# Performance work log

Measured on AMD Instinct MI355X. Metric: run time of the kernel, lower is better.

Reference implementation:

```python
import jax, jax.numpy as jnp
import numpy as np

B, DM, H, W = 2, 96, 48, 48
E = 192          # d_expand == d_inner
R, N = 6, 16     # delta_rank, d_state


def conv2d(x, w, b, groups=1, pad=0):
    out = jax.lax.conv_general_dilated(
        x, w, window_strides=(1, 1), padding=[(pad, pad), (pad, pad)],
        dimension_numbers=("NCHW", "OIHW", "NCHW"), feature_group_count=groups)
    return out + b[None, :, None, None]


def setup_inputs() -> dict:
    key = jax.random.key(0)
    ks = jax.random.split(key, 24)
    f = lambda k, shape, s: jax.random.normal(k, shape, jnp.float32) * s
    inp = {
        "x": jax.random.normal(ks[0], (B, DM, H, W), jnp.float32),
        "in_proj_w": f(ks[1], (2 * E, DM), 0.05),
        "conv_w": f(ks[2], (E, 1, 3, 3), 0.2),
        "conv_b": f(ks[3], (E,), 0.1),
        "x_proj_w": f(ks[4], (4, R + 2 * N, E), 0.01),
        "dt_proj_w": f(ks[5], (4, E, R), 0.01),
        "dt_proj_b": jnp.full((4, E), -9.0) + f(ks[6], (4, E), 0.1),
        "A_log": jnp.tile(jnp.log(jnp.arange(1, N + 1, dtype=jnp.float32))[None, None, :], (4, E, 1)),
        "Ds": jnp.ones((4, E), jnp.float32),
        "ln_g": jnp.ones(E, jnp.float32), "ln_b": jnp.zeros(E, jnp.float32),
        "c1_w": f(ks[7], (2 * E, E, 1, 1), 0.05), "c1_b": jnp.zeros(2 * E),
        "bn1_g": jnp.ones(2 * E), "bn1_b": jnp.zeros(2 * E), "bn1_m": jnp.zeros(2 * E), "bn1_v": jnp.ones(2 * E),
        "c2_w": f(ks[8], (2 * E, 1, 3, 3), 0.2), "c2_b": jnp.zeros(2 * E),
        "bn2_g": jnp.ones(2 * E), "bn2_b": jnp.zeros(2 * E), "bn2_m": jnp.zeros(2 * E), "bn2_v": jnp.ones(2 * E),
        "c3_w": f(ks[9], (E // 2, 2 * E, 1, 1), 0.05), "c3_b": jnp.zeros(E // 2),
        "se1_w": f(ks[10], (E // 4, E // 2), 0.1), "se1_b": jnp.zeros(E // 4),
        "se2_w": f(ks[11], (E // 2, E // 4), 0.1), "se2_b": jnp.zeros(E // 2),
    }
    return inp


def reference(x, in_proj_w, conv_w, conv_b, x_proj_w, dt_proj_w, dt_proj_b,
              A_log, Ds, ln_g, ln_b,
              c1_w, c1_b, bn1_g, bn1_b, bn1_m, bn1_v,
              c2_w, c2_b, bn2_g, bn2_b, bn2_m, bn2_v,
              c3_w, c3_b, se1_w, se1_b, se2_w, se2_b):
    Bs, _, Hs, Ws = x.shape
    L = Hs * Ws
    # in projection (Linear over channel dim), split x/z gates
    xz = jnp.einsum("bchw,oc->bohw", x, in_proj_w)
    xi, z = jnp.split(xz, 2, axis=1)
    # depthwise conv + SiLU
    xi = jax.nn.silu(conv2d(xi, conv_w, conv_b, groups=E, pad=1))
    # ---- selective scan (4-direction cross scan, cumsum formulation) ----
    xf = xi.reshape(Bs, E, L)
    xt = jnp.swapaxes(xi, 2, 3).reshape(Bs, E, L)
    xs = jnp.stack([xf, xf[..., ::-1], xt, xt[..., ::-1]], axis=1)  # [B,4,E,L]
    dbc = jnp.einsum("bkcl,krc->bkrl", xs, x_proj_w)                # [B,4,R+2N,L]
    dlt, b, c = dbc[:, :, :R], dbc[:, :, R:R + N], dbc[:, :, R + N:]
    dlt = jnp.einsum("bkrl,kdr->bkdl", dlt, dt_proj_w) + dt_proj_b[None, :, :, None]
    dlt = jax.nn.softplus(dlt)                                      # [B,4,E,L]
    dA = dlt[..., None] * A_log[None, :, :, None, :]                # [B,4,E,L,N]
    phi = jnp.exp(-jnp.cumsum(dA, axis=3))
    dbx = dlt[..., None] * jnp.swapaxes(b, 2, 3)[:, :, None] * xs[..., None]  # [B,4,E,L,N]
    h = phi * jnp.cumsum(dbx / (phi + 1e-12), axis=3)
    y = jnp.einsum("bkdln,bknl->bkdl", h, c) + Ds[None, :, :, None]  # [B,4,E,L]
    # ---- cross merge ----
    y1 = y[:, 0]
    y2 = y[:, 1, :, ::-1]
    y3 = jnp.swapaxes(y[:, 2].reshape(Bs, E, Ws, Hs), 2, 3).reshape(Bs, E, L)
    y4 = jnp.swapaxes(y[:, 3, :, ::-1].reshape(Bs, E, Ws, Hs), 2, 3).reshape(Bs, E, L)
    ys = (y1 + y2 + y3 + y4).reshape(Bs, E, Hs, Ws)
    # layernorm over channels
    yn = jnp.moveaxis(ys, 1, -1)
    mu = yn.mean(-1, keepdims=True)
    var = yn.var(-1, keepdims=True)
    yn = (yn - mu) / jnp.sqrt(var + 1e-5) * ln_g + ln_b
    u = jnp.moveaxis(yn, -1, 1) * z
    # ---- EFFN ----
    def bn(t, g, bb, m, v):
        return (t - m[None, :, None, None]) / jnp.sqrt(v + 1e-5)[None, :, None, None] * g[None, :, None, None] + bb[None, :, None, None]
    t = jax.nn.relu(bn(conv2d(u, c1_w, c1_b), bn1_g, bn1_b, bn1_m, bn1_v))
    t = jax.nn.relu(bn(conv2d(t, c2_w, c2_b, groups=2 * E, pad=1), bn2_g, bn2_b, bn2_m, bn2_v))
    t = conv2d(t, c3_w, c3_b)
    # squeeze-excitation: t + t * sigmoid(fc(relu(fc(avgpool(t)))))
    s = t.mean((2, 3))
    s = jax.nn.relu(s @ se1_w.T + se1_b)
    s = jax.nn.sigmoid(s @ se2_w.T + se2_b)
    return t + t * s[:, :, None, None]
```

## Files before the change

kernel.cpp:

```cpp
#include <hip/hip_runtime.h>
#include <hip/hip_bf16.h>

#define LTOT 2304
#define ECH  192
#define NCH  16
#define CCH  96
#define SCH  24

__device__ __forceinline__ int permS(int k, int l) {
  if (k == 0) return l;
  if (k == 1) return LTOT - 1 - l;
  int m = (k == 2) ? l : (LTOT - 1 - l);
  return (m % 48) * 48 + (m / 48);
}

__device__ __forceinline__ float softplusf(float x) {
  return (x > 20.f) ? x : log1pf(__expf(x));
}

__global__ __launch_bounds__(256) void k1_inproj(const float* __restrict__ x,
                                                 const float* __restrict__ W,
                                                 float* __restrict__ xi_pre,
                                                 float* __restrict__ z) {
  const int l0 = blockIdx.x * 64;
  const int o0 = blockIdx.y * 64;
  const int b  = blockIdx.z;
  __shared__ __align__(16) float xs[64 * 97];
  __shared__ __align__(16) float Wl[96 * 68];
  const int tid = threadIdx.x;
  for (int idx = tid; idx < 96 * 64; idx += 256) {
    int i = idx & 63, c = idx >> 6;
    xs[i * 97 + c] = x[(b * 96 + c) * LTOT + l0 + i];
  }
  for (int idx = tid; idx < 64 * 96; idx += 256) {
    int r = idx / 96, c = idx - r * 96;
    Wl[c * 68 + r] = W[(o0 + r) * 96 + c];
  }
  __syncthreads();
  const int lane = tid & 63, w = tid >> 6;
  const int jj = lane & 15, rq = lane >> 4;
  const int rbase = 16 * w + 4 * rq;
  float acc[4][4];
#pragma unroll
  for (int p = 0; p < 4; ++p)
#pragma unroll
    for (int t = 0; t < 4; ++t) acc[p][t] = 0.f;
#pragma unroll 2
  for (int c = 0; c < 96; ++c) {
    const float4 wv = *(const float4*)&Wl[c * 68 + rbase];
    float xv[4];
#pragma unroll
    for (int p = 0; p < 4; ++p) xv[p] = xs[(jj + 16 * p) * 97 + c];
#pragma unroll
    for (int p = 0; p < 4; ++p) {
      acc[p][0] = fmaf(wv.x, xv[p], acc[p][0]);
      acc[p][1] = fmaf(wv.y, xv[p], acc[p][1]);
      acc[p][2] = fmaf(wv.z, xv[p], acc[p][2]);
      acc[p][3] = fmaf(wv.w, xv[p], acc[p][3]);
    }
  }
  __syncthreads();
  float* ol = xs;
#pragma unroll
  for (int p = 0; p < 4; ++p)
#pragma unroll
    for (int t = 0; t < 4; ++t) ol[(rbase + t) * 65 + jj + 16 * p] = acc[p][t];
  __syncthreads();
  for (int idx = tid; idx < 64 * 64; idx += 256) {
    int r = idx & 63, pos = idx >> 6;
    float v = ol[r * 65 + pos];
    int o = o0 + r, l = l0 + pos;
    if (o < ECH) xi_pre[(b * LTOT + l) * ECH + o] = v;
    else         z[(b * LTOT + l) * ECH + (o - ECH)] = v;
  }
}

__global__ __launch_bounds__(256) void k2_dwconv(const float* __restrict__ xi_pre,
                                                 const float* __restrict__ cw,
                                                 const float* __restrict__ cb,
                                                 float* __restrict__ xi) {
  int g = blockIdx.x * 256 + threadIdx.x;
  if (g >= 2 * LTOT * ECH) return;
  int e = g % ECH; int l = (g / ECH) % LTOT; int b = g / (ECH * LTOT);
  int h = l / 48, wq = l % 48;
  float acc = cb[e];
#pragma unroll
  for (int kh = 0; kh < 3; ++kh) {
    int hh = h + kh - 1; if (hh < 0 || hh >= 48) continue;
#pragma unroll
    for (int kw = 0; kw < 3; ++kw) {
      int ww = wq + kw - 1; if (ww < 0 || ww >= 48) continue;
      acc = fmaf(cw[e * 9 + kh * 3 + kw], xi_pre[(b * LTOT + hh * 48 + ww) * ECH + e], acc);
    }
  }
  xi[g] = acc / (1.f + __expf(-acc));
}

__global__ __launch_bounds__(256) void k3_xproj(const float* __restrict__ xi,
                                                const float* __restrict__ xw,
                                                const float* __restrict__ dtw,
                                                const float* __restrict__ dtb,
                                                float* __restrict__ dlt,
                                                float* __restrict__ bT,
                                                float* __restrict__ cT) {
  const int l0 = blockIdx.x * 32;
  const int k  = blockIdx.y;
  const int b  = blockIdx.z;
  __shared__ __align__(16) float xs[32 * 193];
  __shared__ __align__(16) float Wl[192 * 40];
  __shared__ float dl6[6 * 33];
  const int tid = threadIdx.x;
  for (int idx = tid; idx < 32 * 192; idx += 256) {
    int j = idx / 192, c = idx - j * 192;
    int s = permS(k, l0 + j);
    xs[j * 193 + c] = xi[(b * LTOT + s) * ECH + c];
  }
  const float* wsrc = xw + k * 38 * ECH;
  for (int idx = tid; idx < 38 * 192; idx += 256) {
    int r = idx / 192, c = idx - r * 192;
    Wl[c * 40 + r] = wsrc[idx];
  }
  __syncthreads();
  const int lane = tid & 63, w = tid >> 6;
  const int jj = lane & 15;
  const int rq = w * 4 + (lane >> 4);
  const int rqc = rq < 9 ? rq : 9;
  const int j0 = 2 * jj;
  float a00 = 0.f, a01 = 0.f, a02 = 0.f, a03 = 0.f;
  float a10 = 0.f, a11 = 0.f, a12 = 0.f, a13 = 0.f;
#pragma unroll 4
  for (int c = 0; c < 192; ++c) {
    float x0 = xs[j0 * 193 + c];
    float x1 = xs[j0 * 193 + 193 + c];
    const float4 wv = *(const float4*)&Wl[c * 40 + 4 * rqc];
    a00 = fmaf(wv.x, x0, a00); a01 = fmaf(wv.y, x0, a01);
    a02 = fmaf(wv.z, x0, a02); a03 = fmaf(wv.w, x0, a03);
    a10 = fmaf(wv.x, x1, a10); a11 = fmaf(wv.y, x1, a11);
    a12 = fmaf(wv.z, x1, a12); a13 = fmaf(wv.w, x1, a13);
  }
  const int bk = b * 4 + k;
  if (rq < 10) {
    float av[2][4] = {{a00, a01, a02, a03}, {a10, a11, a12, a13}};
#pragma unroll
    for (int t = 0; t < 4; ++t) {
      int r = 4 * rq + t;
      if (r >= 38) continue;
#pragma unroll
      for (int p = 0; p < 2; ++p) {
        int j = j0 + p;
        float v = av[p][t];
        if (r < 6)       dl6[r * 33 + j] = v;
        else if (r < 22) bT[((bk * LTOT) + l0 + j) * NCH + (r - 6)] = v;
        else             cT[((bk * LTOT) + l0 + j) * NCH + (r - 22)] = v;
      }
    }
  }
  __syncthreads();
  for (int idx = tid; idx < 32 * 192; idx += 256) {
    int j = idx / 192, d = idx - j * 192;
    float a = dtb[k * ECH + d];
    const float* wd = dtw + (k * ECH + d) * 6;
#pragma unroll
    for (int r = 0; r < 6; ++r) a = fmaf(wd[r], dl6[r * 33 + j], a);
    dlt[((bk * LTOT) + l0 + j) * ECH + d] = softplusf(a);
  }
}

__global__ __launch_bounds__(256) void k4a_scan1(const float* __restrict__ dlt,
                                                 const float* __restrict__ xi,
                                                 const float* __restrict__ bT,
                                                 const float* __restrict__ Alog,
                                                 float* __restrict__ q,
                                                 float* __restrict__ Ts) {
  const int cb = blockIdx.x;
  const int db = blockIdx.y;
  const int bk = blockIdx.z;
  const int b = bk >> 2, k = bk & 3;
  const int l0 = cb * 96;
  __shared__ float sdl[96 * 64];
  __shared__ float sxi[96 * 64];
  __shared__ __align__(16) float sb[96 * NCH];
  const int tid = threadIdx.x;
  const int dd = tid & 63, cg = tid >> 6;
  const int dg = db * 64 + dd;
  for (int j = cg; j < 96; j += 4) {
    sdl[j * 64 + dd] = dlt[(bk * LTOT + l0 + j) * ECH + dg];
    int s = permS(k, l0 + j);
    sxi[j * 64 + dd] = xi[(b * LTOT + s) * ECH + dg];
  }
  for (int idx = tid; idx < 96 * NCH; idx += 256) sb[idx] = bT[(bk * LTOT + l0) * NCH + idx];
  __syncthreads();
  float C1[16], C2[16], C3[16], h[16];
#pragma unroll
  for (int n = 0; n < 16; ++n) {
    float a = Alog[(k * ECH + dg) * NCH + n];
    C1[n] = a; C2[n] = 0.5f * a * a; C3[n] = (1.f / 6.f) * a * a * a;
    h[n] = 0.f;
  }
  float Tsum = 0.f;
  const int c = cb * 4 + cg;
  for (int i = 0; i < SCH; ++i) {
    int j = cg * SCH + i;
    float dl = sdl[j * 64 + dd];
    float u  = dl * sxi[j * 64 + dd];
    Tsum += dl;
    const float4* bb4 = (const float4*)(sb + j * NCH);
    float4 q0 = bb4[0], q1 = bb4[1], q2 = bb4[2], q3 = bb4[3];
    float bbl[16] = {q0.x, q0.y, q0.z, q0.w, q1.x, q1.y, q1.z, q1.w,
                     q2.x, q2.y, q2.z, q2.w, q3.x, q3.y, q3.z, q3.w};
    if (dl <= 0.018f) {
#pragma unroll
      for (int n = 0; n < 16; ++n) {
        float e = fmaf(dl, fmaf(dl, fmaf(dl, -C3[n], C2[n]), -C1[n]), 1.f);
        h[n] = fmaf(e, h[n], u * bbl[n]);
      }
    } else {
#pragma unroll
      for (int n = 0; n < 16; ++n) {
        float e = __expf(-C1[n] * dl);
        h[n] = fmaf(e, h[n], u * bbl[n]);
      }
    }
  }
  float* qp = q + ((bk * CCH + c) * ECH + dg) * NCH;
#pragma unroll
  for (int n = 0; n < 16; ++n) qp[n] = h[n];
  Ts[(bk * CCH + c) * ECH + dg] = Tsum;
}

__global__ __launch_bounds__(256) void k4b_comb(const float* __restrict__ Alog,
                                                const float* __restrict__ Ts,
                                                float* __restrict__ q) {
  int t = blockIdx.x * 256 + threadIdx.x;
  if (t >= 8 * ECH * NCH) return;
  int n = t & 15, d = (t >> 4) % ECH, bk = t / (NCH * ECH);
  int k = bk & 3;
  float A = Alog[(k * ECH + d) * NCH + n];
  float h = 0.f;
  for (int c = 0; c < CCH; ++c) {
    int base = ((bk * CCH + c) * ECH + d) * NCH + n;
    float qc = q[base];
    q[base] = h;
    float xv = A * Ts[(bk * CCH + c) * ECH + d];
    float P = (xv <= 0.05f)
                  ? fmaf(xv, fmaf(xv, fmaf(xv, -(1.f / 6.f), 0.5f), -1.f), 1.f)
                  : __expf(-xv);
    h = fmaf(P, h, qc);
  }
}

__global__ __launch_bounds__(256) void k4c_scan2(const float* __restrict__ dlt,
                                                 const float* __restrict__ xi,
                                                 const float* __restrict__ bT,
                                                 const float* __restrict__ cT,
                                                 const float* __restrict__ Alog,
                                                 const float* __restrict__ hin,
                                                 float* __restrict__ ys) {
  const int cb = blockIdx.x;
  const int db = blockIdx.y;
  const int bk = blockIdx.z;
  const int b = bk >> 2, k = bk & 3;
  const int l0 = cb * 96;
  __shared__ float sdl[96 * 64];
  __shared__ float sxi[96 * 64];
  __shared__ __align__(16) float sb[96 * NCH];
  __shared__ __align__(16) float sc[96 * NCH];
  const int tid = threadIdx.x;
  const int dd = tid & 63, cg = tid >> 6;
  const int dg = db * 64 + dd;
  for (int j = cg; j < 96; j += 4) {
    sdl[j * 64 + dd] = dlt[(bk * LTOT + l0 + j) * ECH + dg];
    int s = permS(k, l0 + j);
    sxi[j * 64 + dd] = xi[(b * LTOT + s) * ECH + dg];
  }
  for (int idx = tid; idx < 96 * NCH; idx += 256) {
    sb[idx] = bT[(bk * LTOT + l0) * NCH + idx];
    sc[idx] = cT[(bk * LTOT + l0) * NCH + idx];
  }
  __syncthreads();
  float C1[16], C2[16], C3[16], h[16];
  const int c = cb * 4 + cg;
  const float* hp = hin + ((bk * CCH + c) * ECH + dg) * NCH;
#pragma unroll
  for (int n = 0; n < 16; ++n) {
    float a = Alog[(k * ECH + dg) * NCH + n];
    C1[n] = a; C2[n] = 0.5f * a * a; C3[n] = (1.f / 6.f) * a * a * a;
    h[n] = hp[n];
  }
  for (int i = 0; i < SCH; ++i) {
    int j = cg * SCH + i;
    int l = l0 + j;
    float dl = sdl[j * 64 + dd];
    float u  = dl * sxi[j * 64 + dd];
    const float4* bb4 = (const float4*)(sb + j * NCH);
    float4 q0 = bb4[0], q1 = bb4[1], q2 = bb4[2], q3 = bb4[3];
    float bbl[16] = {q0.x, q0.y, q0.z, q0.w, q1.x, q1.y, q1.z, q1.w,
                     q2.x, q2.y, q2.z, q2.w, q3.x, q3.y, q3.z, q3.w};
    if (dl <= 0.018f) {
#pragma unroll
      for (int n = 0; n < 16; ++n) {
        float e = fmaf(dl, fmaf(dl, fmaf(dl, -C3[n], C2[n]), -C1[n]), 1.f);
        h[n] = fmaf(e, h[n], u * bbl[n]);
      }
    } else {
#pragma unroll
      for (int n = 0; n < 16; ++n) {
        float e = __expf(-C1[n] * dl);
        h[n] = fmaf(e, h[n], u * bbl[n]);
      }
    }
    const float4* cc4 = (const float4*)(sc + j * NCH);
    float4 c0 = cc4[0], c1 = cc4[1], c2 = cc4[2], c3 = cc4[3];
    float ccl[16] = {c0.x, c0.y, c0.z, c0.w, c1.x, c1.y, c1.z, c1.w,
                     c2.x, c2.y, c2.z, c2.w, c3.x, c3.y, c3.z, c3.w};
    float y = 0.f;
#pragma unroll
    for (int n = 0; n < 16; ++n) y = fmaf(h[n], ccl[n], y);
    int s = permS(k, l);
    atomicAdd(&ys[(b * LTOT + s) * ECH + dg], y);
  }
}

__global__ __launch_bounds__(256) void k5_ln(const float* __restrict__ ys,
                                             const float* __restrict__ Ds,
                                             const float* __restrict__ lng,
                                             const float* __restrict__ lnb,
                                             float* __restrict__ zu) {
  int p = blockIdx.x * 4 + (threadIdx.x >> 6);
  int lane = threadIdx.x & 63;
  const float* yp = ys + p * ECH;
  float vd[3], sd[3];
#pragma unroll
  for (int t = 0; t < 3; ++t) {
    int d = lane + t * 64;
    vd[t] = yp[d];
    sd[t] = Ds[d] + Ds[ECH + d] + Ds[2 * ECH + d] + Ds[3 * ECH + d];
  }
  float s1 = vd[0] + vd[1] + vd[2];
  float s2 = sd[0] + sd[1] + sd[2];
#pragma unroll
  for (int off = 32; off > 0; off >>= 1) {
    s1 += __shfl_xor(s1, off, 64);
    s2 += __shfl_xor(s2, off, 64);
  }
  float mean_dot = s1 * (1.f / 192.f);
  float mean_sd  = s2 * (1.f / 192.f);
  float dev[3];
  float ss = 0.f;
#pragma unroll
  for (int t = 0; t < 3; ++t) {
    dev[t] = (vd[t] - mean_dot) + (sd[t] - mean_sd);
    ss = fmaf(dev[t], dev[t], ss);
  }
#pragma unroll
  for (int off = 32; off > 0; off >>= 1) ss += __shfl_xor(ss, off, 64);
  float rstd = 1.f / sqrtf(ss * (1.f / 192.f) + 1e-5f);
#pragma unroll
  for (int t = 0; t < 3; ++t) {
    int d = lane + t * 64;
    float yn = (dev[t] * rstd) * lng[d] + lnb[d];
    zu[p * ECH + d] = yn * zu[p * ECH + d];
  }
}

__global__ __launch_bounds__(256) void k6_c1(const float* __restrict__ u,
                                             const float* __restrict__ W,
                                             const float* __restrict__ c1b,
                                             const float* __restrict__ g1,
                                             const float* __restrict__ b1,
                                             const float* __restrict__ m1,
                                             const float* __restrict__ v1,
                                             float* __restrict__ t1) {
  const int l0 = blockIdx.x * 64;
  const int o0 = blockIdx.y * 64;
  const int b  = blockIdx.z;
  __shared__ __align__(16) float xs[64 * 97];
  __shared__ __align__(16) float Wl[96 * 68];
  const int tid = threadIdx.x;
  const int lane = tid & 63, w = tid >> 6;
  const int jj = lane & 15, rq = lane >> 4;
  const int rbase = 16 * w + 4 * rq;
  float acc[4][4];
#pragma unroll
  for (int p = 0; p < 4; ++p)
#pragma unroll
    for (int t = 0; t < 4; ++t) acc[p][t] = 0.f;
  for (int kc = 0; kc < 2; ++kc) {
    if (kc) __syncthreads();
    for (int idx = tid; idx < 64 * 96; idx += 256) {
      int i = idx / 96, c = idx - i * 96;
      xs[i * 97 + c] = u[(b * LTOT + l0 + i) * ECH + kc * 96 + c];
    }
    for (int idx = tid; idx < 64 * 96; idx += 256) {
      int r = idx / 96, c = idx - r * 96;
      Wl[c * 68 + r] = W[(o0 + r) * ECH + kc * 96 + c];
    }
    __syncthreads();
#pragma unroll 2
    for (int c = 0; c < 96; ++c) {
      const float4 wv = *(const float4*)&Wl[c * 68 + rbase];
      float xv[4];
#pragma unroll
      for (int p = 0; p < 4; ++p) xv[p] = xs[(jj + 16 * p) * 97 + c];
#pragma unroll
      for (int p = 0; p < 4; ++p) {
        acc[p][0] = fmaf(wv.x, xv[p], acc[p][0]);
        acc[p][1] = fmaf(wv.y, xv[p], acc[p][1]);
        acc[p][2] = fmaf(wv.z, xv[p], acc[p][2]);
        acc[p][3] = fmaf(wv.w, xv[p], acc[p][3]);
      }
    }
  }
#pragma unroll
  for (int t = 0; t < 4; ++t) {
    int o = o0 + rbase + t;
    float sc = g1[o] / sqrtf(v1[o] + 1e-5f);
    float bias = (c1b[o] - m1[o]) * sc + b1[o];
#pragma unroll
    for (int p = 0; p < 4; ++p) acc[p][t] = fmaxf(fmaf(acc[p][t], sc, bias), 0.f);
  }
  __syncthreads();
  float* ol = xs;
#pragma unroll
  for (int p = 0; p < 4; ++p)
#pragma unroll
    for (int t = 0; t < 4; ++t) ol[(rbase + t) * 65 + jj + 16 * p] = acc[p][t];
  __syncthreads();
  for (int idx = tid; idx < 64 * 64; idx += 256) {
    int pos = idx & 63, r = idx >> 6;
    t1[(b * 384 + o0 + r) * LTOT + l0 + pos] = ol[r * 65 + pos];
  }
}

__global__ __launch_bounds__(256) void k7_dw2(const float* __restrict__ t1,
                                              const float* __restrict__ cw,
                                              const float* __restrict__ cb,
                                              const float* __restrict__ g2,
                                              const float* __restrict__ b2,
                                              const float* __restrict__ m2,
                                              const float* __restrict__ v2,
                                              float* __restrict__ t2) {
  int g = blockIdx.x * 256 + threadIdx.x;
  if (g >= 2 * LTOT * 384) return;
  int l = g % LTOT; int o = (g / LTOT) % 384; int b = g / (LTOT * 384);
  int h = l / 48, wq = l % 48;
  const float* src = t1 + (b * 384 + o) * LTOT;
  float acc = cb[o];
#pragma unroll
  for (int kh = 0; kh < 3; ++kh) {
    int hh = h + kh - 1; if (hh < 0 || hh >= 48) continue;
#pragma unroll
    for (int kw = 0; kw < 3; ++kw) {
      int ww = wq + kw - 1; if (ww < 0 || ww >= 48) continue;
      acc = fmaf(cw[o * 9 + kh * 3 + kw], src[hh * 48 + ww], acc);
    }
  }
  float sc = g2[o] / sqrtf(v2[o] + 1e-5f);
  float val = (acc - m2[o]) * sc + b2[o];
  t2[g] = fmaxf(val, 0.f);
}

__global__ __launch_bounds__(256) void k8_c3(const float* __restrict__ t2,
                                             const float* __restrict__ W,
                                             const float* __restrict__ c3b,
                                             float* __restrict__ t3,
                                             float* __restrict__ se) {
  const int l0 = blockIdx.x * 64;
  const int r0 = blockIdx.y * 32;
  const int b  = blockIdx.z;
  __shared__ __align__(16) float xs[64 * 97];
  __shared__ __align__(16) float Wl[96 * 36];
  const int tid = threadIdx.x;
  const int lane = tid & 63, w = tid >> 6;
  const int jj = lane & 15, rq = lane >> 4;
  const int rloc = 8 * w + 2 * rq;
  float acc[4][2];
#pragma unroll
  for (int p = 0; p < 4; ++p) { acc[p][0] = 0.f; acc[p][1] = 0.f; }
  for (int kc = 0; kc < 4; ++kc) {
    if (kc) __syncthreads();
    for (int idx = tid; idx < 64 * 96; idx += 256) {
      int i = idx & 63, c = idx >> 6;
      xs[i * 97 + c] = t2[(b * 384 + kc * 96 + c) * LTOT + l0 + i];
    }
    for (int idx = tid; idx < 32 * 96; idx += 256) {
      int r = idx / 96, c = idx - r * 96;
      Wl[c * 36 + r] = W[(r0 + r) * 384 + kc * 96 + c];
    }
    __syncthreads();
#pragma unroll 2
    for (int c = 0; c < 96; ++c) {
      const float2 wv = *(const float2*)&Wl[c * 36 + rloc];
      float xv[4];
#pragma unroll
      for (int p = 0; p < 4; ++p) xv[p] = xs[(jj + 16 * p) * 97 + c];
#pragma unroll
      for (int p = 0; p < 4; ++p) {
        acc[p][0] = fmaf(wv.x, xv[p], acc[p][0]);
        acc[p][1] = fmaf(wv.y, xv[p], acc[p][1]);
      }
    }
  }
#pragma unroll
  for (int t = 0; t < 2; ++t) {
    float bias = c3b[r0 + rloc + t];
#pragma unroll
    for (int p = 0; p < 4; ++p) acc[p][t] += bias;
  }
#pragma unroll
  for (int t = 0; t < 2; ++t) {
    float v = acc[0][t] + acc[1][t] + acc[2][t] + acc[3][t];
    v += __shfl_xor(v, 1); v += __shfl_xor(v, 2);
    v += __shfl_xor(v, 4); v += __shfl_xor(v, 8);
    if (jj == 0) atomicAdd(&se[b * 96 + r0 + rloc + t], v);
  }
  __syncthreads();
  float* ol = xs;
#pragma unroll
  for (int p = 0; p < 4; ++p)
#pragma unroll
    for (int t = 0; t < 2; ++t) ol[(rloc + t) * 65 + jj + 16 * p] = acc[p][t];
  __syncthreads();
  for (int idx = tid; idx < 32 * 64; idx += 256) {
    int pos = idx & 63, r = idx >> 6;
    t3[(b * 96 + r0 + r) * LTOT + l0 + pos] = ol[r * 65 + pos];
  }
}

__global__ __launch_bounds__(256) void k9a_se(const float* __restrict__ se,
                                              const float* __restrict__ w1,
                                              const float* __restrict__ sb1,
                                              const float* __restrict__ w2,
                                              const float* __restrict__ sb2,
                                              float* __restrict__ smul) {
  __shared__ float sm[192];
  __shared__ float s1[96];
  int t = threadIdx.x;
  if (t < 192) sm[t] = se[t] * (1.f / 2304.f);
  __syncthreads();
  if (t < 96) {
    int b = t / 48, i = t % 48;
    float acc = sb1[i];
    for (int m = 0; m < 96; ++m) acc = fmaf(w1[i * 96 + m], sm[b * 96 + m], acc);
    s1[t] = fmaxf(acc, 0.f);
  }
  __syncthreads();
  if (t < 192) {
    int b = t / 96, j = t % 96;
    float acc = sb2[j];
    for (int i = 0; i < 48; ++i) acc = fmaf(w2[j * 48 + i], s1[b * 48 + i], acc);
    smul[t] = 1.f + 1.f / (1.f + __expf(-acc));
  }
}

__global__ __launch_bounds__(256) void k9b_out(const float* __restrict__ t3,
                                               const float* __restrict__ smul,
                                               float* __restrict__ out) {
  int g = blockIdx.x * 256 + threadIdx.x;
  if (g >= 2 * 96 * LTOT) return;
  int bj = g / LTOT;
  out[g] = t3[g] * smul[bj];
}

extern "C" void kernel_launch(void* const* d_in, const int* in_sizes, int n_in,
                              void* d_out, int out_size, void* d_ws, size_t ws_size,
                              hipStream_t stream) {
  const float* x     = (const float*)d_in[0];
  const float* inw   = (const float*)d_in[1];
  const float* convw = (const float*)d_in[2];
  const float* convb = (const float*)d_in[3];
  const float* xpw   = (const float*)d_in[4];
  const float* dtw   = (const float*)d_in[5];
  const float* dtb   = (const float*)d_in[6];
  const float* Alog  = (const float*)d_in[7];
  const float* Ds    = (const float*)d_in[8];
  const float* lng   = (const float*)d_in[9];
  const float* lnb   = (const float*)d_in[10];
  const float* c1w   = (const float*)d_in[11];
  const float* c1b   = (const float*)d_in[12];
  const float* bn1g  = (const float*)d_in[13];
  const float* bn1b  = (const float*)d_in[14];
  const float* bn1m  = (const float*)d_in[15];
  const float* bn1v  = (const float*)d_in[16];
  const float* c2w   = (const float*)d_in[17];
  const float* c2b   = (const float*)d_in[18];
  const float* bn2g  = (const float*)d_in[19];
  const float* bn2b  = (const float*)d_in[20];
  const float* bn2m  = (const float*)d_in[21];
  const float* bn2v  = (const float*)d_in[22];
  const float* c3w   = (const float*)d_in[23];
  const float* c3b   = (const float*)d_in[24];
  const float* se1w  = (const float*)d_in[25];
  const float* se1b  = (const float*)d_in[26];
  const float* se2w  = (const float*)d_in[27];
  const float* se2b  = (const float*)d_in[28];

  float* ws = (float*)d_ws;
  float* xi_pre = ws;
  float* z      = ws + 884736;
  float* xi     = ws + 1769472;
  float* dlt    = ws + 2654208;
  float* bT     = ws + 6193152;
  float* cT     = ws + 6782976;
  float* ys     = ws + 7372800;
  float* q      = ws + 8257536;
  float* Ts     = ws + 10616832;
  float* se     = ws + 10764288;
  float* smul   = ws + 10764480;
  float* t1 = dlt;
  float* t2 = dlt + 1769472;
  float* t3 = cT;

  hipMemsetAsync(ys, 0, 884736 * sizeof(float), stream);
  hipMemsetAsync(se, 0, 192 * sizeof(float), stream);

  k1_inproj<<<dim3(36, 6, 2), 256, 0, stream>>>(x, inw, xi_pre, z);
  k2_dwconv<<<3456, 256, 0, stream>>>(xi_pre, convw, convb, xi);
  k3_xproj<<<dim3(72, 4, 2), 256, 0, stream>>>(xi, xpw, dtw, dtb, dlt, bT, cT);
  k4a_scan1<<<dim3(24, 3, 8), 256, 0, stream>>>(dlt, xi, bT, Alog, q, Ts);
  k4b_comb<<<96, 256, 0, stream>>>(Alog, Ts, q);
  k4c_scan2<<<dim3(24, 3, 8), 256, 0, stream>>>(dlt, xi, bT, cT, Alog, q, ys);
  k5_ln<<<1152, 256, 0, stream>>>(ys, Ds, lng, lnb, z);
  k6_c1<<<dim3(36, 6, 2), 256, 0, stream>>>(z, c1w, c1b, bn1g, bn1b, bn1m, bn1v, t1);
  k7_dw2<<<6912, 256, 0, stream>>>(t1, c2w, c2b, bn2g, bn2b, bn2m, bn2v, t2);
  k8_c3<<<dim3(36, 3, 2), 256, 0, stream>>>(t2, c3w, c3b, t3, se);
  k9a_se<<<1, 256, 0, stream>>>(se, se1w, se1b, se2w, se2b, smul);
  k9b_out<<<1728, 256, 0, stream>>>(t3, smul, (float*)d_out);
}
```

Baseline: 349.4 us.

## Recompute delta in scan kernels, drop memsets, transpose GEMM smem tiles

The x-projection kernel now writes only the rank-6 delta inputs. Both scan kernels recompute dt_proj plus softplus on the fly instead of reading a full [B,4,L,E] delta tensor, which cuts a large global write and two reads. The scan now writes per-direction outputs (yd) rather than atomically accumulating into a zeroed ys, so the ys memset goes away, and the SE accumulator is zeroed inside k6. The GEMM kernels switch their shared-memory input tiles to a channel-major layout with float2 loads, and q/h are moved with float4. The cost is redundant softplus and exp work across the two scan passes and a changed scan staging scheme split into halves.

```diff
diff --git a/kernel.cpp b/kernel.cpp
--- a/kernel.cpp
+++ b/kernel.cpp
@@ -14,8 +14,9 @@
   return (m % 48) * 48 + (m / 48);
 }
 
-__device__ __forceinline__ float softplusf(float x) {
-  return (x > 20.f) ? x : log1pf(__expf(x));
+__device__ __forceinline__ float sp_fast(float x) {
+  float t = __expf(x);
+  return (t <= 0.018f) ? t * fmaf(t, fmaf(t, 0.33333334f, -0.5f), 1.f) : log1pf(t);
 }
 
 __global__ __launch_bounds__(256) void k1_inproj(const float* __restrict__ x,
@@ -25,46 +26,49 @@
   const int l0 = blockIdx.x * 64;
   const int o0 = blockIdx.y * 64;
   const int b  = blockIdx.z;
-  __shared__ __align__(16) float xs[64 * 97];
+  __shared__ __align__(16) float xs[96 * 66];
   __shared__ __align__(16) float Wl[96 * 68];
   const int tid = threadIdx.x;
   for (int idx = tid; idx < 96 * 64; idx += 256) {
-    int i = idx & 63, c = idx >> 6;
-    xs[i * 97 + c] = x[(b * 96 + c) * LTOT + l0 + i];
+    int i = idx & 63, cc = idx >> 6;
+    xs[cc * 66 + i] = x[(b * 96 + cc) * LTOT + l0 + i];
   }
   for (int idx = tid; idx < 64 * 96; idx += 256) {
-    int r = idx / 96, c = idx - r * 96;
-    Wl[c * 68 + r] = W[(o0 + r) * 96 + c];
+    int r = idx / 96, cc = idx - r * 96;
+    Wl[cc * 68 + r] = W[(o0 + r) * 96 + cc];
   }
   __syncthreads();
   const int lane = tid & 63, w = tid >> 6;
-  const int jj = lane & 15, rq = lane >> 4;
-  const int rbase = 16 * w + 4 * rq;
+  const int jj = lane & 15, rqq = lane >> 4;
+  const int rbase = 16 * w + 4 * rqq;
   float acc[4][4];
 #pragma unroll
   for (int p = 0; p < 4; ++p)
 #pragma unroll
     for (int t = 0; t < 4; ++t) acc[p][t] = 0.f;
 #pragma unroll 2
-  for (int c = 0; c < 96; ++c) {
-    const float4 wv = *(const float4*)&Wl[c * 68 + rbase];
-    float xv[4];
-#pragma unroll
-    for (int p = 0; p < 4; ++p) xv[p] = xs[(jj + 16 * p) * 97 + c];
-#pragma unroll
-    for (int p = 0; p < 4; ++p) {
-      acc[p][0] = fmaf(wv.x, xv[p], acc[p][0]);
-      acc[p][1] = fmaf(wv.y, xv[p], acc[p][1]);
-      acc[p][2] = fmaf(wv.z, xv[p], acc[p][2]);
-      acc[p][3] = fmaf(wv.w, xv[p], acc[p][3]);
-    }
+  for (int cc = 0; cc < 96; ++cc) {
+    const float4 wv = *(const float4*)&Wl[cc * 68 + rbase];
+    const float2 xa = *(const float2*)&xs[cc * 66 + 2 * jj];
+    const float2 xb = *(const float2*)&xs[cc * 66 + 32 + 2 * jj];
+    acc[0][0] = fmaf(wv.x, xa.x, acc[0][0]); acc[0][1] = fmaf(wv.y, xa.x, acc[0][1]);
+    acc[0][2] = fmaf(wv.z, xa.x, acc[0][2]); acc[0][3] = fmaf(wv.w, xa.x, acc[0][3]);
+    acc[1][0] = fmaf(wv.x, xa.y, acc[1][0]); acc[1][1] = fmaf(wv.y, xa.y, acc[1][1]);
+    acc[1][2] = fmaf(wv.z, xa.y, acc[1][2]); acc[1][3] = fmaf(wv.w, xa.y, acc[1][3]);
+    acc[2][0] = fmaf(wv.x, xb.x, acc[2][0]); acc[2][1] = fmaf(wv.y, xb.x, acc[2][1]);
+    acc[2][2] = fmaf(wv.z, xb.x, acc[2][2]); acc[2][3] = fmaf(wv.w, xb.x, acc[2][3]);
+    acc[3][0] = fmaf(wv.x, xb.y, acc[3][0]); acc[3][1] = fmaf(wv.y, xb.y, acc[3][1]);
+    acc[3][2] = fmaf(wv.z, xb.y, acc[3][2]); acc[3][3] = fmaf(wv.w, xb.y, acc[3][3]);
   }
   __syncthreads();
   float* ol = xs;
 #pragma unroll
-  for (int p = 0; p < 4; ++p)
-#pragma unroll
-    for (int t = 0; t < 4; ++t) ol[(rbase + t) * 65 + jj + 16 * p] = acc[p][t];
+  for (int t = 0; t < 4; ++t) {
+    ol[(rbase + t) * 65 + 2 * jj]      = acc[0][t];
+    ol[(rbase + t) * 65 + 2 * jj + 1]  = acc[1][t];
+    ol[(rbase + t) * 65 + 2 * jj + 32] = acc[2][t];
+    ol[(rbase + t) * 65 + 2 * jj + 33] = acc[3][t];
+  }
   __syncthreads();
   for (int idx = tid; idx < 64 * 64; idx += 256) {
     int r = idx & 63, pos = idx >> 6;
@@ -98,29 +102,20 @@
 
 __global__ __launch_bounds__(256) void k3_xproj(const float* __restrict__ xi,
                                                 const float* __restrict__ xw,
-                                                const float* __restrict__ dtw,
-                                                const float* __restrict__ dtb,
-                                                float* __restrict__ dlt,
+                                                float* __restrict__ dl6g,
                                                 float* __restrict__ bT,
                                                 float* __restrict__ cT) {
   const int l0 = blockIdx.x * 32;
   const int k  = blockIdx.y;
   const int b  = blockIdx.z;
-  __shared__ __align__(16) float xs[32 * 193];
+  __shared__ __align__(16) float xs[96 * 34];
   __shared__ __align__(16) float Wl[192 * 40];
-  __shared__ float dl6[6 * 33];
   const int tid = threadIdx.x;
-  for (int idx = tid; idx < 32 * 192; idx += 256) {
-    int j = idx / 192, c = idx - j * 192;
-    int s = permS(k, l0 + j);
-    xs[j * 193 + c] = xi[(b * LTOT + s) * ECH + c];
-  }
   const float* wsrc = xw + k * 38 * ECH;
   for (int idx = tid; idx < 38 * 192; idx += 256) {
-    int r = idx / 192, c = idx - r * 192;
-    Wl[c * 40 + r] = wsrc[idx];
-  }
-  __syncthreads();
+    int r = idx / 192, cc = idx - r * 192;
+    Wl[cc * 40 + r] = wsrc[idx];
+  }
   const int lane = tid & 63, w = tid >> 6;
   const int jj = lane & 15;
   const int rq = w * 4 + (lane >> 4);
@@ -128,15 +123,23 @@
   const int j0 = 2 * jj;
   float a00 = 0.f, a01 = 0.f, a02 = 0.f, a03 = 0.f;
   float a10 = 0.f, a11 = 0.f, a12 = 0.f, a13 = 0.f;
+  for (int kc = 0; kc < 2; ++kc) {
+    __syncthreads();
+    for (int idx = tid; idx < 32 * 96; idx += 256) {
+      int j = idx / 96, cc = idx - j * 96;
+      int s = permS(k, l0 + j);
+      xs[cc * 34 + j] = xi[(b * LTOT + s) * ECH + kc * 96 + cc];
+    }
+    __syncthreads();
 #pragma unroll 4
-  for (int c = 0; c < 192; ++c) {
-    float x0 = xs[j0 * 193 + c];
-    float x1 = xs[j0 * 193 + 193 + c];
-    const float4 wv = *(const float4*)&Wl[c * 40 + 4 * rqc];
-    a00 = fmaf(wv.x, x0, a00); a01 = fmaf(wv.y, x0, a01);
-    a02 = fmaf(wv.z, x0, a02); a03 = fmaf(wv.w, x0, a03);
-    a10 = fmaf(wv.x, x1, a10); a11 = fmaf(wv.y, x1, a11);
-    a12 = fmaf(wv.z, x1, a12); a13 = fmaf(wv.w, x1, a13);
+    for (int cc = 0; cc < 96; ++cc) {
+      const float2 xv = *(const float2*)&xs[cc * 34 + j0];
+      const float4 wv = *(const float4*)&Wl[(kc * 96 + cc) * 40 + 4 * rqc];
+      a00 = fmaf(wv.x, xv.x, a00); a01 = fmaf(wv.y, xv.x, a01);
+      a02 = fmaf(wv.z, xv.x, a02); a03 = fmaf(wv.w, xv.x, a03);
+      a10 = fmaf(wv.x, xv.y, a10); a11 = fmaf(wv.y, xv.y, a11);
+      a12 = fmaf(wv.z, xv.y, a12); a13 = fmaf(wv.w, xv.y, a13);
+    }
   }
   const int bk = b * 4 + k;
   if (rq < 10) {
@@ -149,27 +152,20 @@
       for (int p = 0; p < 2; ++p) {
         int j = j0 + p;
         float v = av[p][t];
-        if (r < 6)       dl6[r * 33 + j] = v;
+        if (r < 6)       dl6g[((bk * LTOT) + l0 + j) * 6 + r] = v;
         else if (r < 22) bT[((bk * LTOT) + l0 + j) * NCH + (r - 6)] = v;
         else             cT[((bk * LTOT) + l0 + j) * NCH + (r - 22)] = v;
       }
     }
   }
-  __syncthreads();
-  for (int idx = tid; idx < 32 * 192; idx += 256) {
-    int j = idx / 192, d = idx - j * 192;
-    float a = dtb[k * ECH + d];
-    const float* wd = dtw + (k * ECH + d) * 6;
-#pragma unroll
-    for (int r = 0; r < 6; ++r) a = fmaf(wd[r], dl6[r * 33 + j], a);
-    dlt[((bk * LTOT) + l0 + j) * ECH + d] = softplusf(a);
-  }
-}
-
-__global__ __launch_bounds__(256) void k4a_scan1(const float* __restrict__ dlt,
+}
+
+__global__ __launch_bounds__(256) void k4a_scan1(const float* __restrict__ dl6g,
                                                  const float* __restrict__ xi,
                                                  const float* __restrict__ bT,
                                                  const float* __restrict__ Alog,
+                                                 const float* __restrict__ dtw,
+                                                 const float* __restrict__ dtb,
                                                  float* __restrict__ q,
                                                  float* __restrict__ Ts) {
   const int cb = blockIdx.x;
@@ -177,54 +173,75 @@
   const int bk = blockIdx.z;
   const int b = bk >> 2, k = bk & 3;
   const int l0 = cb * 96;
-  __shared__ float sdl[96 * 64];
-  __shared__ float sxi[96 * 64];
-  __shared__ __align__(16) float sb[96 * NCH];
+  __shared__ __align__(16) float2 sdx[48 * 64];
+  __shared__ __align__(16) float  sb[96 * NCH];
+  __shared__ __align__(16) float  sdl6[96 * 6];
   const int tid = threadIdx.x;
   const int dd = tid & 63, cg = tid >> 6;
   const int dg = db * 64 + dd;
-  for (int j = cg; j < 96; j += 4) {
-    sdl[j * 64 + dd] = dlt[(bk * LTOT + l0 + j) * ECH + dg];
-    int s = permS(k, l0 + j);
-    sxi[j * 64 + dd] = xi[(b * LTOT + s) * ECH + dg];
-  }
+  float b6 = dtb[k * ECH + dg];
+  float w6[6];
+  {
+    const float2* d2 = (const float2*)(dtw + (k * ECH + dg) * 6);
+    float2 u0 = d2[0], u1 = d2[1], u2 = d2[2];
+    w6[0] = u0.x; w6[1] = u0.y; w6[2] = u1.x; w6[3] = u1.y; w6[4] = u2.x; w6[5] = u2.y;
+  }
+  for (int idx = tid; idx < 96 * 6; idx += 256) sdl6[idx] = dl6g[(bk * LTOT + l0) * 6 + idx];
   for (int idx = tid; idx < 96 * NCH; idx += 256) sb[idx] = bT[(bk * LTOT + l0) * NCH + idx];
-  __syncthreads();
-  float C1[16], C2[16], C3[16], h[16];
+  float C1[16], h[16];
 #pragma unroll
   for (int n = 0; n < 16; ++n) {
-    float a = Alog[(k * ECH + dg) * NCH + n];
-    C1[n] = a; C2[n] = 0.5f * a * a; C3[n] = (1.f / 6.f) * a * a * a;
+    C1[n] = Alog[(k * ECH + dg) * NCH + n];
     h[n] = 0.f;
   }
   float Tsum = 0.f;
   const int c = cb * 4 + cg;
-  for (int i = 0; i < SCH; ++i) {
-    int j = cg * SCH + i;
-    float dl = sdl[j * 64 + dd];
-    float u  = dl * sxi[j * 64 + dd];
-    Tsum += dl;
-    const float4* bb4 = (const float4*)(sb + j * NCH);
-    float4 q0 = bb4[0], q1 = bb4[1], q2 = bb4[2], q3 = bb4[3];
-    float bbl[16] = {q0.x, q0.y, q0.z, q0.w, q1.x, q1.y, q1.z, q1.w,
-                     q2.x, q2.y, q2.z, q2.w, q3.x, q3.y, q3.z, q3.w};
-    if (dl <= 0.018f) {
-#pragma unroll
-      for (int n = 0; n < 16; ++n) {
-        float e = fmaf(dl, fmaf(dl, fmaf(dl, -C3[n], C2[n]), -C1[n]), 1.f);
-        h[n] = fmaf(e, h[n], u * bbl[n]);
+  for (int half = 0; half < 2; ++half) {
+    __syncthreads();
+    for (int e = tid; e < 48 * 64; e += 256) {
+      int s = e >> 6;
+      int j = (s / 12) * 24 + half * 12 + (s % 12);
+      const float* d6 = sdl6 + j * 6;
+      float xa = b6;
+#pragma unroll
+      for (int r = 0; r < 6; ++r) xa = fmaf(w6[r], d6[r], xa);
+      float dl = sp_fast(xa);
+      int sp = permS(k, l0 + j);
+      float xiv = xi[(b * LTOT + sp) * ECH + dg];
+      sdx[s * 64 + dd] = make_float2(dl, xiv);
+    }
+    __syncthreads();
+    for (int i = 0; i < 12; ++i) {
+      int j = cg * 24 + half * 12 + i;
+      float2 dx = sdx[(cg * 12 + i) * 64 + dd];
+      float dl = dx.x;
+      float u  = dl * dx.y;
+      Tsum += dl;
+      const float4* bb4 = (const float4*)(sb + j * NCH);
+      float4 q0 = bb4[0], q1 = bb4[1], q2 = bb4[2], q3 = bb4[3];
+      float bbl[16] = {q0.x, q0.y, q0.z, q0.w, q1.x, q1.y, q1.z, q1.w,
+                       q2.x, q2.y, q2.z, q2.w, q3.x, q3.y, q3.z, q3.w};
+      if (dl <= 0.018f) {
+#pragma unroll
+        for (int n = 0; n < 16; ++n) {
+          float xn = C1[n] * dl;
+          float e = fmaf(xn, fmaf(xn, fmaf(xn, -(1.f / 6.f), 0.5f), -1.f), 1.f);
+          h[n] = fmaf(e, h[n], u * bbl[n]);
+        }
+      } else {
+#pragma unroll
+        for (int n = 0; n < 16; ++n) {
+          float e = __expf(-C1[n] * dl);
+          h[n] = fmaf(e, h[n], u * bbl[n]);
+        }
       }
-    } else {
-#pragma unroll
-      for (int n = 0; n < 16; ++n) {
-        float e = __expf(-C1[n] * dl);
-        h[n] = fmaf(e, h[n], u * bbl[n]);
-      }
-    }
-  }
-  float* qp = q + ((bk * CCH + c) * ECH + dg) * NCH;
-#pragma unroll
-  for (int n = 0; n < 16; ++n) qp[n] = h[n];
+    }
+  }
+  float4* qp = (float4*)(q + ((bk * CCH + c) * ECH + dg) * NCH);
+  qp[0] = make_float4(h[0], h[1], h[2], h[3]);
+  qp[1] = make_float4(h[4], h[5], h[6], h[7]);
+  qp[2] = make_float4(h[8], h[9], h[10], h[11]);
+  qp[3] = make_float4(h[12], h[13], h[14], h[15]);
   Ts[(bk * CCH + c) * ECH + dg] = Tsum;
 }
 
@@ -249,91 +266,118 @@
   }
 }
 
-__global__ __launch_bounds__(256) void k4c_scan2(const float* __restrict__ dlt,
+__global__ __launch_bounds__(256) void k4c_scan2(const float* __restrict__ dl6g,
                                                  const float* __restrict__ xi,
                                                  const float* __restrict__ bT,
                                                  const float* __restrict__ cT,
                                                  const float* __restrict__ Alog,
+                                                 const float* __restrict__ dtw,
+                                                 const float* __restrict__ dtb,
                                                  const float* __restrict__ hin,
-                                                 float* __restrict__ ys) {
+                                                 float* __restrict__ yd) {
   const int cb = blockIdx.x;
   const int db = blockIdx.y;
   const int bk = blockIdx.z;
   const int b = bk >> 2, k = bk & 3;
   const int l0 = cb * 96;
-  __shared__ float sdl[96 * 64];
-  __shared__ float sxi[96 * 64];
-  __shared__ __align__(16) float sb[96 * NCH];
-  __shared__ __align__(16) float sc[96 * NCH];
+  __shared__ __align__(16) float2 sdx[48 * 64];
+  __shared__ __align__(16) float  sb[96 * NCH];
+  __shared__ __align__(16) float  sc[96 * NCH];
+  __shared__ __align__(16) float  sdl6[96 * 6];
   const int tid = threadIdx.x;
   const int dd = tid & 63, cg = tid >> 6;
   const int dg = db * 64 + dd;
-  for (int j = cg; j < 96; j += 4) {
-    sdl[j * 64 + dd] = dlt[(bk * LTOT + l0 + j) * ECH + dg];
-    int s = permS(k, l0 + j);
-    sxi[j * 64 + dd] = xi[(b * LTOT + s) * ECH + dg];
-  }
+  float b6 = dtb[k * ECH + dg];
+  float w6[6];
+  {
+    const float2* d2 = (const float2*)(dtw + (k * ECH + dg) * 6);
+    float2 u0 = d2[0], u1 = d2[1], u2 = d2[2];
+    w6[0] = u0.x; w6[1] = u0.y; w6[2] = u1.x; w6[3] = u1.y; w6[4] = u2.x; w6[5] = u2.y;
+  }
+  for (int idx = tid; idx < 96 * 6; idx += 256) sdl6[idx] = dl6g[(bk * LTOT + l0) * 6 + idx];
   for (int idx = tid; idx < 96 * NCH; idx += 256) {
     sb[idx] = bT[(bk * LTOT + l0) * NCH + idx];
     sc[idx] = cT[(bk * LTOT + l0) * NCH + idx];
   }
-  __syncthreads();
-  float C1[16], C2[16], C3[16], h[16];
+  float C1[16], h[16];
   const int c = cb * 4 + cg;
-  const float* hp = hin + ((bk * CCH + c) * ECH + dg) * NCH;
-#pragma unroll
-  for (int n = 0; n < 16; ++n) {
-    float a = Alog[(k * ECH + dg) * NCH + n];
-    C1[n] = a; C2[n] = 0.5f * a * a; C3[n] = (1.f / 6.f) * a * a * a;
-    h[n] = hp[n];
-  }
-  for (int i = 0; i < SCH; ++i) {
-    int j = cg * SCH + i;
-    int l = l0 + j;
-    float dl = sdl[j * 64 + dd];
-    float u  = dl * sxi[j * 64 + dd];
-    const float4* bb4 = (const float4*)(sb + j * NCH);
-    float4 q0 = bb4[0], q1 = bb4[1], q2 = bb4[2], q3 = bb4[3];
-    float bbl[16] = {q0.x, q0.y, q0.z, q0.w, q1.x, q1.y, q1.z, q1.w,
-                     q2.x, q2.y, q2.z, q2.w, q3.x, q3.y, q3.z, q3.w};
-    if (dl <= 0.018f) {
-#pragma unroll
-      for (int n = 0; n < 16; ++n) {
-        float e = fmaf(dl, fmaf(dl, fmaf(dl, -C3[n], C2[n]), -C1[n]), 1.f);
-        h[n] = fmaf(e, h[n], u * bbl[n]);
+  const float4* hp = (const float4*)(hin + ((bk * CCH + c) * ECH + dg) * NCH);
+  {
+    float4 h0 = hp[0], h1 = hp[1], h2 = hp[2], h3 = hp[3];
+    h[0]=h0.x; h[1]=h0.y; h[2]=h0.z; h[3]=h0.w;
+    h[4]=h1.x; h[5]=h1.y; h[6]=h1.z; h[7]=h1.w;
+    h[8]=h2.x; h[9]=h2.y; h[10]=h2.z; h[11]=h2.w;
+    h[12]=h3.x; h[13]=h3.y; h[14]=h3.z; h[15]=h3.w;
+  }
+#pragma unroll
+  for (int n = 0; n < 16; ++n) C1[n] = Alog[(k * ECH + dg) * NCH + n];
+  float* ydk = yd + (b * 4 + k) * LTOT * ECH;
+  for (int half = 0; half < 2; ++half) {
+    __syncthreads();
+    for (int e = tid; e < 48 * 64; e += 256) {
+      int s = e >> 6;
+      int j = (s / 12) * 24 + half * 12 + (s % 12);
+      const float* d6 = sdl6 + j * 6;
+      float xa = b6;
+#pragma unroll
+      for (int r = 0; r < 6; ++r) xa = fmaf(w6[r], d6[r], xa);
+      float dl = sp_fast(xa);
+      int sp = permS(k, l0 + j);
+      float xiv = xi[(b * LTOT + sp) * ECH + dg];
+      sdx[s * 64 + dd] = make_float2(dl, xiv);
+    }
+    __syncthreads();
+    for (int i = 0; i < 12; ++i) {
+      int j = cg * 24 + half * 12 + i;
+      float2 dx = sdx[(cg * 12 + i) * 64 + dd];
+      float dl = dx.x;
+      float u  = dl * dx.y;
+      const float4* bb4 = (const float4*)(sb + j * NCH);
+      float4 q0 = bb4[0], q1 = bb4[1], q2 = bb4[2], q3 = bb4[3];
+      float bbl[16] = {q0.x, q0.y, q0.z, q0.w, q1.x, q1.y, q1.z, q1.w,
+                       q2.x, q2.y, q2.z, q2.w, q3.x, q3.y, q3.z, q3.w};
+      if (dl <= 0.018f) {
+#pragma unroll
+        for (int n = 0; n < 16; ++n) {
+          float xn = C1[n] * dl;
+          float e = fmaf(xn, fmaf(xn, fmaf(xn, -(1.f / 6.f), 0.5f), -1.f), 1.f);
+          h[n] = fmaf(e, h[n], u * bbl[n]);
+        }
+      } else {
+#pragma unroll
+        for (int n = 0; n < 16; ++n) {
+          float e = __expf(-C1[n] * dl);
+          h[n] = fmaf(e, h[n], u * bbl[n]);
+        }
       }
-    } else {
-#pragma unroll
-      for (int n = 0; n < 16; ++n) {
-        float e = __expf(-C1[n] * dl);
-        h[n] = fmaf(e, h[n], u * bbl[n]);
-      }
-    }
-    const float4* cc4 = (const float4*)(sc + j * NCH);
-    float4 c0 = cc4[0], c1 = cc4[1], c2 = cc4[2], c3 = cc4[3];
-    float ccl[16] = {c0.x, c0.y, c0.z, c0.w, c1.x, c1.y, c1.z, c1.w,
-                     c2.x, c2.y, c2.z, c2.w, c3.x, c3.y, c3.z, c3.w};
-    float y = 0.f;
-#pragma unroll
-    for (int n = 0; n < 16; ++n) y = fmaf(h[n], ccl[n], y);
-    int s = permS(k, l);
-    atomicAdd(&ys[(b * LTOT + s) * ECH + dg], y);
-  }
-}
-
-__global__ __launch_bounds__(256) void k5_ln(const float* __restrict__ ys,
+      const float4* cc4 = (const float4*)(sc + j * NCH);
+      float4 c0 = cc4[0], c1 = cc4[1], c2 = cc4[2], c3 = cc4[3];
+      float ccl[16] = {c0.x, c0.y, c0.z, c0.w, c1.x, c1.y, c1.z, c1.w,
+                       c2.x, c2.y, c2.z, c2.w, c3.x, c3.y, c3.z, c3.w};
+      float y = 0.f;
+#pragma unroll
+      for (int n = 0; n < 16; ++n) y = fmaf(h[n], ccl[n], y);
+      int sp = permS(k, l0 + j);
+      ydk[sp * ECH + dg] = y;
+    }
+  }
+}
+
+__global__ __launch_bounds__(256) void k5_ln(const float* __restrict__ yd,
                                              const float* __restrict__ Ds,
                                              const float* __restrict__ lng,
                                              const float* __restrict__ lnb,
                                              float* __restrict__ zu) {
   int p = blockIdx.x * 4 + (threadIdx.x >> 6);
   int lane = threadIdx.x & 63;
-  const float* yp = ys + p * ECH;
+  int b = (p >= LTOT) ? 1 : 0;
+  int l = p - b * LTOT;
+  const float* y0 = yd + (b * 4) * LTOT * ECH + l * ECH;
   float vd[3], sd[3];
 #pragma unroll
   for (int t = 0; t < 3; ++t) {
     int d = lane + t * 64;
-    vd[t] = yp[d];
+    vd[t] = ((y0[d] + y0[LTOT * ECH + d]) + y0[2 * LTOT * ECH + d]) + y0[3 * LTOT * ECH + d];
     sd[t] = Ds[d] + Ds[ECH + d] + Ds[2 * ECH + d] + Ds[3 * ECH + d];
   }
   float s1 = vd[0] + vd[1] + vd[2];
@@ -370,16 +414,18 @@
                                              const float* __restrict__ b1,
                                              const float* __restrict__ m1,
                                              const float* __restrict__ v1,
-                                             float* __restrict__ t1) {
+                                             float* __restrict__ t1,
+                                             float* __restrict__ se) {
   const int l0 = blockIdx.x * 64;
   const int o0 = blockIdx.y * 64;
   const int b  = blockIdx.z;
-  __shared__ __align__(16) float xs[64 * 97];
+  const int tid = threadIdx.x;
+  if (blockIdx.x == 0 && blockIdx.y == 0 && blockIdx.z == 0 && tid < 192) se[tid] = 0.f;
+  __shared__ __align__(16) float xs[96 * 66];
   __shared__ __align__(16) float Wl[96 * 68];
-  const int tid = threadIdx.x;
   const int lane = tid & 63, w = tid >> 6;
-  const int jj = lane & 15, rq = lane >> 4;
-  const int rbase = 16 * w + 4 * rq;
+  const int jj = lane & 15, rqq = lane >> 4;
+  const int rbase = 16 * w + 4 * rqq;
   float acc[4][4];
 #pragma unroll
   for (int p = 0; p < 4; ++p)
@@ -388,27 +434,27 @@
   for (int kc = 0; kc < 2; ++kc) {
     if (kc) __syncthreads();
     for (int idx = tid; idx < 64 * 96; idx += 256) {
-      int i = idx / 96, c = idx - i * 96;
-      xs[i * 97 + c] = u[(b * LTOT + l0 + i) * ECH + kc * 96 + c];
+      int i = idx / 96, cc = idx - i * 96;
+      xs[cc * 66 + i] = u[(b * LTOT + l0 + i) * ECH + kc * 96 + cc];
     }
     for (int idx = tid; idx < 64 * 96; idx += 256) {
-      int r = idx / 96, c = idx - r * 96;
-      Wl[c * 68 + r] = W[(o0 + r) * ECH + kc * 96 + c];
+      int r = idx / 96, cc = idx - r * 96;
+      Wl[cc * 68 + r] = W[(o0 + r) * ECH + kc * 96 + cc];
     }
     __syncthreads();
 #pragma unroll 2
-    for (int c = 0; c < 96; ++c) {
-      const float4 wv = *(const float4*)&Wl[c * 68 + rbase];
-      float xv[4];
-#pragma unroll
-      for (int p = 0; p < 4; ++p) xv[p] = xs[(jj + 16 * p) * 97 + c];
-#pragma unroll
-      for (int p = 0; p < 4; ++p) {
-        acc[p][0] = fmaf(wv.x, xv[p], acc[p][0]);
-        acc[p][1] = fmaf(wv.y, xv[p], acc[p][1]);
-        acc[p][2] = fmaf(wv.z, xv[p], acc[p][2]);
-        acc[p][3] = fmaf(wv.w, xv[p], acc[p][3]);
-      }
+    for (int cc = 0; cc < 96; ++cc) {
+      const float4 wv = *(const float4*)&Wl[cc * 68 + rbase];
+      const float2 xa = *(const float2*)&xs[cc * 66 + 2 * jj];
+      const float2 xb = *(const float2*)&xs[cc * 66 + 32 + 2 * jj];
+      acc[0][0] = fmaf(wv.x, xa.x, acc[0][0]); acc[0][1] = fmaf(wv.y, xa.x, acc[0][1]);
+      acc[0][2] = fmaf(wv.z, xa.x, acc[0][2]); acc[0][3] = fmaf(wv.w, xa.x, acc[0][3]);
+      acc[1][0] = fmaf(wv.x, xa.y, acc[1][0]); acc[1][1] = fmaf(wv.y, xa.y, acc[1][1]);
+      acc[1][2] = fmaf(wv.z, xa.y, acc[1][2]); acc[1][3] = fmaf(wv.w, xa.y, acc[1][3]);
+      acc[2][0] = fmaf(wv.x, xb.x, acc[2][0]); acc[2][1] = fmaf(wv.y, xb.x, acc[2][1]);
+      acc[2][2] = fmaf(wv.z, xb.x, acc[2][2]); acc[2][3] = fmaf(wv.w, xb.x, acc[2][3]);
+      acc[3][0] = fmaf(wv.x, xb.y, acc[3][0]); acc[3][1] = fmaf(wv.y, xb.y, acc[3][1]);
+      acc[3][2] = fmaf(wv.z, xb.y, acc[3][2]); acc[3][3] = fmaf(wv.w, xb.y, acc[3][3]);
     }
   }
 #pragma unroll
@@ -422,9 +468,12 @@
   __syncthreads();
   float* ol = xs;
 #pragma unroll
-  for (int p = 0; p < 4; ++p)
-#pragma unroll
-    for (int t = 0; t < 4; ++t) ol[(rbase + t) * 65 + jj + 16 * p] = acc[p][t];
+  for (int t = 0; t < 4; ++t) {
+    ol[(rbase + t) * 65 + 2 * jj]      = acc[0][t];
+    ol[(rbase + t) * 65 + 2 * jj + 1]  = acc[1][t];
+    ol[(rbase + t) * 65 + 2 * jj + 32] = acc[2][t];
+    ol[(rbase + t) * 65 + 2 * jj + 33] = acc[3][t];
+  }
   __syncthreads();
   for (int idx = tid; idx < 64 * 64; idx += 256) {
     int pos = idx & 63, r = idx >> 6;
@@ -468,37 +517,35 @@
   const int l0 = blockIdx.x * 64;
   const int r0 = blockIdx.y * 32;
   const int b  = blockIdx.z;
-  __shared__ __align__(16) float xs[64 * 97];
+  __shared__ __align__(16) float xs[96 * 66];
   __shared__ __align__(16) float Wl[96 * 36];
   const int tid = threadIdx.x;
   const int lane = tid & 63, w = tid >> 6;
-  const int jj = lane & 15, rq = lane >> 4;
-  const int rloc = 8 * w + 2 * rq;
+  const int jj = lane & 15, rqq = lane >> 4;
+  const int rloc = 8 * w + 2 * rqq;
   float acc[4][2];
 #pragma unroll
   for (int p = 0; p < 4; ++p) { acc[p][0] = 0.f; acc[p][1] = 0.f; }
   for (int kc = 0; kc < 4; ++kc) {
     if (kc) __syncthreads();
     for (int idx = tid; idx < 64 * 96; idx += 256) {
-      int i = idx & 63, c = idx >> 6;
-      xs[i * 97 + c] = t2[(b * 384 + kc * 96 + c) * LTOT + l0 + i];
+      int i = idx & 63, cc = idx >> 6;
+      xs[cc * 66 + i] = t2[(b * 384 + kc * 96 + cc) * LTOT + l0 + i];
     }
     for (int idx = tid; idx < 32 * 96; idx += 256) {
-      int r = idx / 96, c = idx - r * 96;
-      Wl[c * 36 + r] = W[(r0 + r) * 384 + kc * 96 + c];
+      int r = idx / 96, cc = idx - r * 96;
+      Wl[cc * 36 + r] = W[(r0 + r) * 384 + kc * 96 + cc];
     }
     __syncthreads();
 #pragma unroll 2
-    for (int c = 0; c < 96; ++c) {
-      const float2 wv = *(const float2*)&Wl[c * 36 + rloc];
-      float xv[4];
-#pragma unroll
-      for (int p = 0; p < 4; ++p) xv[p] = xs[(jj + 16 * p) * 97 + c];
-#pragma unroll
-      for (int p = 0; p < 4; ++p) {
-        acc[p][0] = fmaf(wv.x, xv[p], acc[p][0]);
-        acc[p][1] = fmaf(wv.y, xv[p], acc[p][1]);
-      }
+    for (int cc = 0; cc < 96; ++cc) {
+      const float2 wv = *(const float2*)&Wl[cc * 36 + rloc];
+      const float2 xa = *(const float2*)&xs[cc * 66 + 2 * jj];
+      const float2 xb = *(const float2*)&xs[cc * 66 + 32 + 2 * jj];
+      acc[0][0] = fmaf(wv.x, xa.x, acc[0][0]); acc[0][1] = fmaf(wv.y, xa.x, acc[0][1]);
+      acc[1][0] = fmaf(wv.x, xa.y, acc[1][0]); acc[1][1] = fmaf(wv.y, xa.y, acc[1][1]);
+      acc[2][0] = fmaf(wv.x, xb.x, acc[2][0]); acc[2][1] = fmaf(wv.y, xb.x, acc[2][1]);
+      acc[3][0] = fmaf(wv.x, xb.y, acc[3][0]); acc[3][1] = fmaf(wv.y, xb.y, acc[3][1]);
     }
   }
 #pragma unroll
@@ -517,9 +564,12 @@
   __syncthreads();
   float* ol = xs;
 #pragma unroll
-  for (int p = 0; p < 4; ++p)
-#pragma unroll
-    for (int t = 0; t < 2; ++t) ol[(rloc + t) * 65 + jj + 16 * p] = acc[p][t];
+  for (int t = 0; t < 2; ++t) {
+    ol[(rloc + t) * 65 + 2 * jj]      = acc[0][t];
+    ol[(rloc + t) * 65 + 2 * jj + 1]  = acc[1][t];
+    ol[(rloc + t) * 65 + 2 * jj + 32] = acc[2][t];
+    ol[(rloc + t) * 65 + 2 * jj + 33] = acc[3][t];
+  }
   __syncthreads();
   for (int idx = tid; idx < 32 * 64; idx += 256) {
     int pos = idx & 63, r = idx >> 6;
@@ -599,29 +649,26 @@
   float* xi_pre = ws;
   float* z      = ws + 884736;
   float* xi     = ws + 1769472;
-  float* dlt    = ws + 2654208;
-  float* bT     = ws + 6193152;
-  float* cT     = ws + 6782976;
-  float* ys     = ws + 7372800;
-  float* q      = ws + 8257536;
-  float* Ts     = ws + 10616832;
-  float* se     = ws + 10764288;
-  float* smul   = ws + 10764480;
-  float* t1 = dlt;
-  float* t2 = dlt + 1769472;
-  float* t3 = cT;
-
-  hipMemsetAsync(ys, 0, 884736 * sizeof(float), stream);
-  hipMemsetAsync(se, 0, 192 * sizeof(float), stream);
+  float* dl6g   = ws + 2654208;
+  float* bT     = ws + 2764800;
+  float* cT     = ws + 3354624;
+  float* q      = ws + 3944448;
+  float* Ts     = ws + 6303744;
+  float* se     = ws + 6451200;
+  float* smul   = ws + 6451392;
+  float* yd     = ws + 6451584;
+  float* t1 = yd;
+  float* t2 = yd + 1769472;
+  float* t3 = q;
 
   k1_inproj<<<dim3(36, 6, 2), 256, 0, stream>>>(x, inw, xi_pre, z);
   k2_dwconv<<<3456, 256, 0, stream>>>(xi_pre, convw, convb, xi);
-  k3_xproj<<<dim3(72, 4, 2), 256, 0, stream>>>(xi, xpw, dtw, dtb, dlt, bT, cT);
-  k4a_scan1<<<dim3(24, 3, 8), 256, 0, stream>>>(dlt, xi, bT, Alog, q, Ts);
+  k3_xproj<<<dim3(72, 4, 2), 256, 0, stream>>>(xi, xpw, dl6g, bT, cT);
+  k4a_scan1<<<dim3(24, 3, 8), 256, 0, stream>>>(dl6g, xi, bT, Alog, dtw, dtb, q, Ts);
   k4b_comb<<<96, 256, 0, stream>>>(Alog, Ts, q);
-  k4c_scan2<<<dim3(24, 3, 8), 256, 0, stream>>>(dlt, xi, bT, cT, Alog, q, ys);
-  k5_ln<<<1152, 256, 0, stream>>>(ys, Ds, lng, lnb, z);
-  k6_c1<<<dim3(36, 6, 2), 256, 0, stream>>>(z, c1w, c1b, bn1g, bn1b, bn1m, bn1v, t1);
+  k4c_scan2<<<dim3(24, 3, 8), 256, 0, stream>>>(dl6g, xi, bT, cT, Alog, dtw, dtb, q, yd);
+  k5_ln<<<1152, 256, 0, stream>>>(yd, Ds, lng, lnb, z);
+  k6_c1<<<dim3(36, 6, 2), 256, 0, stream>>>(z, c1w, c1b, bn1g, bn1b, bn1m, bn1v, t1, se);
   k7_dw2<<<6912, 256, 0, stream>>>(t1, c2w, c2b, bn2g, bn2b, bn2m, bn2v, t2);
   k8_c3<<<dim3(36, 3, 2), 256, 0, stream>>>(t2, c3w, c3b, t3, se);
   k9a_se<<<1, 256, 0, stream>>>(se, se1w, se1b, se2w, se2b, smul);
```

New measurement: 329.1 us. -5.8%, faster.
